# Kernel tuning notes

Measured on AMD Instinct MI355X. Metric: run time of the kernel, lower is better.

The kernel has to match this reference:

```python
import jax, jax.numpy as jnp
import numpy as np

N_HEADS = 8
N_POINTS = 4
EPS = 1e-5


def _conv1x1(x, w, b):
    # x: [B,C,H,W], w: [O,C]
    return jnp.einsum('bchw,oc->bohw', x, w) + b[None, :, None, None]


def _gn(x, g, b, groups=32):
    B, C, H, W = x.shape
    xr = x.reshape(B, groups, C // groups, H, W)
    m = xr.mean((2, 3, 4), keepdims=True)
    v = xr.var((2, 3, 4), keepdims=True)
    xn = ((xr - m) * jax.lax.rsqrt(v + EPS)).reshape(B, C, H, W)
    return xn * g[None, :, None, None] + b[None, :, None, None]


def _ln(x, g, b):
    m = x.mean(-1, keepdims=True)
    v = x.var(-1, keepdims=True)
    return (x - m) * jax.lax.rsqrt(v + EPS) * g + b


def _ln_spec(x, g2, b2, n):
    # modality-specific LayerNorm: separate params for v tokens [:n] and i tokens [n:]
    return jnp.concatenate([_ln(x[:, :n], g2[0], b2[0]), _ln(x[:, n:], g2[1], b2[1])], 1)


def _sine_pos(h, w, d):
    nf = d // 2
    scale = 2.0 * np.pi
    ye = jnp.arange(1, h + 1, dtype=jnp.float32) / h * scale
    xe = jnp.arange(1, w + 1, dtype=jnp.float32) / w * scale
    dim_t = 10000.0 ** (2.0 * (jnp.arange(nf) // 2).astype(jnp.float32) / nf)
    def enc(e):
        p = e[:, None] / dim_t
        return jnp.stack([jnp.sin(p[:, 0::2]), jnp.cos(p[:, 1::2])], -1).reshape(e.shape[0], nf)
    py = enc(ye)  # [h,nf]
    px = enc(xe)  # [w,nf]
    pos = jnp.concatenate([jnp.broadcast_to(py[:, None, :], (h, w, nf)),
                           jnp.broadcast_to(px[None, :, :], (h, w, nf))], -1)
    return pos.reshape(h * w, d)


def _bilinear(vl, loc):
    # vl: [B,h,w,Hd,Dh] value for one level, loc: [B,Lq,Hd,P,2] normalized (x,y)
    B, h, w, Hd, Dh = vl.shape
    Lq, P = loc.shape[1], loc.shape[3]
    x = loc[..., 0] * w - 0.5
    y = loc[..., 1] * h - 0.5
    x0 = jnp.floor(x)
    y0 = jnp.floor(y)
    wx = x - x0
    wy = y - y0
    x0i = x0.astype(jnp.int32)
    y0i = y0.astype(jnp.int32)
    v2 = vl.reshape(B, h * w, Hd, Dh).transpose(0, 2, 1, 3)  # [B,Hd,HW,Dh]
    def g(ix, iy):
        valid = ((ix >= 0) & (ix < w) & (iy >= 0) & (iy < h)).astype(vl.dtype)
        flat = jnp.clip(iy, 0, h - 1) * w + jnp.clip(ix, 0, w - 1)  # [B,Lq,Hd,P]
        idx = flat.transpose(0, 2, 1, 3).reshape(B, Hd, Lq * P)
        gv = jnp.take_along_axis(v2, idx[..., None], axis=2)  # [B,Hd,Lq*P,Dh]
        gv = gv.reshape(B, Hd, Lq, P, Dh).transpose(0, 2, 1, 3, 4)  # [B,Lq,Hd,P,Dh]
        return gv * valid[..., None]
    return (g(x0i, y0i) * ((1 - wx) * (1 - wy))[..., None]
            + g(x0i + 1, y0i) * (wx * (1 - wy))[..., None]
            + g(x0i, y0i + 1) * ((1 - wx) * wy)[..., None]
            + g(x0i + 1, y0i + 1) * (wx * wy)[..., None])


def _deform_attn(q, src, ref, shapes, ow, ob, aww, awb, vw, vb, opw, opb):
    B, Len, D = src.shape
    L = len(shapes)
    Hd, P = N_HEADS, N_POINTS
    Dh = D // Hd
    value = src @ vw + vb
    off = (q @ ow + ob).reshape(B, Len, Hd, L, P, 2)
    aw = jax.nn.softmax((q @ aww + awb).reshape(B, Len, Hd, L * P), -1).reshape(B, Len, Hd, L, P)
    norm = jnp.array([[s[1], s[0]] for s in shapes], jnp.float32)  # (w,h) per level
    loc = ref[None, :, None, None, None, :] + off / norm[None, None, None, :, None, :]
    out = jnp.zeros((B, Len, Hd, Dh), value.dtype)
    start = 0
    for l, (hh, ww) in enumerate(shapes):
        vl = value[:, start:start + hh * ww].reshape(B, hh, ww, Hd, Dh)
        samp = _bilinear(vl, loc[:, :, :, l])  # [B,Len,Hd,P,Dh]
        out = out + (samp * aw[:, :, :, l, :, None]).sum(3)
        start += hh * ww
    return out.reshape(B, Len, D) @ opw + opb


def _forward(input_v, input_i, av_w, av_b, av_g, av_be, ai_w, ai_b, ai_g, ai_be,
             level_embed, off_w, off_b, aw_w, aw_b, vp_w, vp_b, op_w, op_b,
             ln1_g, ln1_b, ffn1_w, ffn1_b, ffn2_w, ffn2_b, ln2_g, ln2_b,
             as_w, as_b, as_g, as_be):
    b, c, h, w = input_v.shape
    D = av_w.shape[0]
    hw = h * w
    fv = _gn(_conv1x1(input_v, av_w, av_b), av_g, av_be)
    fi = _gn(_conv1x1(input_i, ai_w, ai_b), ai_g, ai_be)
    sv = fv.reshape(b, D, hw).transpose(0, 2, 1)
    si = fi.reshape(b, D, hw).transpose(0, 2, 1)
    src = jnp.concatenate([sv, si], 1)  # [b, 2hw, D]
    pos = _sine_pos(h, w, D)
    posf = jnp.concatenate([pos + level_embed[0], pos + level_embed[1]], 0)
    gx = (jnp.arange(w, dtype=jnp.float32) + 0.5) / w
    gy = (jnp.arange(h, dtype=jnp.float32) + 0.5) / h
    X, Y = jnp.meshgrid(gx, gy)
    ref1 = jnp.stack([X, Y], -1).reshape(hw, 2)
    ref = jnp.concatenate([ref1, ref1], 0)  # [2hw, 2]
    shapes = [(h, w), (h, w)]
    for i in range(off_w.shape[0]):
        q = src + posf
        attn = _deform_attn(q, src, ref, shapes, off_w[i], off_b[i], aw_w[i], aw_b[i],
                            vp_w[i], vp_b[i], op_w[i], op_b[i])
        src = _ln_spec(src + attn, ln1_g[i], ln1_b[i], hw)
        ff = jax.nn.relu(src @ ffn1_w[i] + ffn1_b[i]) @ ffn2_w[i] + ffn2_b[i]
        src = _ln_spec(src + ff, ln2_g[i], ln2_b[i], hw)
    out = src[:, :hw] + src[:, hw:]  # chunk along tokens, sum modalities
    out = out.transpose(0, 2, 1).reshape(b, D, h, w)
    return _gn(_conv1x1(out, as_w, as_b), as_g, as_be)


def setup_inputs():
    key = jax.random.key(0)
    B, C, H, W = 16, 768, 20, 20
    D, NL, Hd, L, P, Dff = 512, 6, N_HEADS, 2, N_POINTS, 1024
    ks = iter(jax.random.split(key, 64))
    def rn(shape, scale=0.02):
        return jax.random.normal(next(ks), shape, jnp.float32) * scale
    return {
        'input_v': jax.random.normal(next(ks), (B, C, H, W), jnp.float32),
        'input_i': jax.random.normal(next(ks), (B, C, H, W), jnp.float32),
        'av_w': rn((D, C)), 'av_b': jnp.zeros((D,)), 'av_g': jnp.ones((D,)), 'av_be': jnp.zeros((D,)),
        'ai_w': rn((D, C)), 'ai_b': jnp.zeros((D,)), 'ai_g': jnp.ones((D,)), 'ai_be': jnp.zeros((D,)),
        'level_embed': rn((L, D)),
        'off_w': rn((NL, D, Hd * L * P * 2)), 'off_b': rn((NL, Hd * L * P * 2), 0.5),
        'aw_w': rn((NL, D, Hd * L * P)), 'aw_b': jnp.zeros((NL, Hd * L * P)),
        'vp_w': rn((NL, D, D)), 'vp_b': jnp.zeros((NL, D)),
        'op_w': rn((NL, D, D)), 'op_b': jnp.zeros((NL, D)),
        'ln1_g': jnp.ones((NL, 2, D)), 'ln1_b': jnp.zeros((NL, 2, D)),
        'ffn1_w': rn((NL, D, Dff)), 'ffn1_b': jnp.zeros((NL, Dff)),
        'ffn2_w': rn((NL, Dff, D)), 'ffn2_b': jnp.zeros((NL, D)),
        'ln2_g': jnp.ones((NL, 2, D)), 'ln2_b': jnp.zeros((NL, 2, D)),
        'as_w': rn((C, D)), 'as_b': jnp.zeros((C,)), 'as_g': jnp.ones((C,)), 'as_be': jnp.zeros((C,)),
    }


def reference(input_v, input_i, av_w, av_b, av_g, av_be, ai_w, ai_b, ai_g, ai_be,
              level_embed, off_w, off_b, aw_w, aw_b, vp_w, vp_b, op_w, op_b,
              ln1_g, ln1_b, ffn1_w, ffn1_b, ffn2_w, ffn2_b, ln2_g, ln2_b,
              as_w, as_b, as_g, as_be):
    return _forward(input_v, input_i, av_w, av_b, av_g, av_be, ai_w, ai_b, ai_g, ai_be,
                    level_embed, off_w, off_b, aw_w, aw_b, vp_w, vp_b, op_w, op_b,
                    ln1_g, ln1_b, ffn1_w, ffn1_b, ffn2_w, ffn2_b, ln2_g, ln2_b,
                    as_w, as_b, as_g, as_be)
```

## Files before the change

### kernel.cpp

```cpp
#include <hip/hip_runtime.h>
#include <hip/hip_bf16.h>
#include <cstddef>
#include <math.h>


constexpr int kB   = 16;
constexpr int kCin = 768;
constexpr int kHW  = 400;
constexpr int kWpx = 20;
constexpr int kHpx = 20;
constexpr int kD   = 512;
constexpr int kLen = 800;
constexpr int kDff = 1024;
constexpr int kNL  = 6;
constexpr float kEps = 1e-5f;

typedef __attribute__((ext_vector_type(8))) short s8v;
typedef __attribute__((ext_vector_type(4))) short s4v;
typedef __attribute__((ext_vector_type(4))) float f4v;

__device__ __forceinline__ int swzk(int row, int k) {
  return (k & ~31) | ((((k >> 3) + (row >> 1)) & 3) << 3) | (k & 7);
}

__device__ __forceinline__ unsigned short f2b(float f) {
  union { __hip_bfloat16 h; unsigned short u; } cv;
  cv.h = __float2bfloat16(f);
  return cv.u;
}

__device__ __forceinline__ float b2f(unsigned short u) {
  return __uint_as_float(((unsigned)u) << 16);
}

__device__ __forceinline__ void gll(const unsigned short* g, unsigned short* l) {
  __builtin_amdgcn_global_load_lds(
      (const __attribute__((address_space(1))) unsigned int*)g,
      (__attribute__((address_space(3))) unsigned int*)l, 16, 0, 0);
}

__device__ __forceinline__ void breduce2(float& s, float& s2, float* sh) {
#pragma unroll
  for (int o = 32; o > 0; o >>= 1) {
    s  += __shfl_down(s, o);
    s2 += __shfl_down(s2, o);
  }
  const int wid = threadIdx.x >> 6, lane = threadIdx.x & 63;
  if (lane == 0) { sh[wid] = s; sh[4 + wid] = s2; }
  __syncthreads();
  if (threadIdx.x == 0) {
    sh[0] = sh[0] + sh[1] + sh[2] + sh[3];
    sh[4] = sh[4] + sh[5] + sh[6] + sh[7];
  }
  __syncthreads();
  s = sh[0]; s2 = sh[4];
}

template<int EPI>
__global__ __launch_bounds__(256)
void mgemm(const unsigned short* __restrict__ Abf,
           const unsigned short* __restrict__ Bw,
           const float* __restrict__ bias,
           const unsigned short* __restrict__ resb,
           float* __restrict__ Cf, float* __restrict__ Cf2,
           const float* __restrict__ aux,
           unsigned short* __restrict__ Cb,
           int K, int ldc, int Nreal)
{
  __shared__ unsigned short As[3][4096];
  __shared__ unsigned short Bs[3][4096];
  const int tid = threadIdx.x;
  const int w = tid >> 6, l = tid & 63;
  const int m0 = blockIdx.y * 128;
  const int n0 = blockIdx.x * 128;

  if (EPI == 6 && m0 >= 6400) { Bw = resb; bias = aux; }

  f4v acc[4][4] = {};

  const int srow = w * 32 + (l >> 2);
  const unsigned short* ga0 = Abf + (size_t)(m0 + srow) * K + (l & 3) * 8;
  const unsigned short* ga1 = ga0 + (size_t)16 * K;
  const unsigned short* gb0 = Bw + (size_t)(n0 + srow) * K + (l & 3) * 8;
  const unsigned short* gb1 = gb0 + (size_t)16 * K;
  const int lb0 = (w * 32) * 32;
  const int lb1 = (w * 32 + 16) * 32;

  int aoff[4], boff[4];
#pragma unroll
  for (int f = 0; f < 4; f++) {
    const int ra = (w >> 1) * 64 + f * 16 + (l & 15);
    aoff[f] = ra * 32 + ((((l >> 4) + (ra >> 1)) & 3) << 3);
    const int rb = (w & 1) * 64 + f * 16 + (l & 15);
    boff[f] = rb * 32 + ((((l >> 4) + (rb >> 1)) & 3) << 3);
  }

#define STAGE(ko, bi) do { \
    gll(ga0 + (ko), &As[bi][lb0]); gll(ga1 + (ko), &As[bi][lb1]); \
    gll(gb0 + (ko), &Bs[bi][lb0]); gll(gb1 + (ko), &Bs[bi][lb1]); } while (0)

  const int NT = K >> 5;
  STAGE(0, 0);
  STAGE(32, 1);

  int cur = 0;
  int bpre = 2;
  int kpre = 64;
  for (int t = 0; t < NT; ++t) {
    if (t + 1 < NT) asm volatile("s_waitcnt vmcnt(4)" ::: "memory");
    else            asm volatile("s_waitcnt vmcnt(0)" ::: "memory");
    __builtin_amdgcn_s_barrier();
    __builtin_amdgcn_sched_barrier(0);
    if (t + 2 < NT) STAGE(kpre, bpre);
    s8v af[4], bf4[4];
#pragma unroll
    for (int f = 0; f < 4; f++) {
      af[f]  = *(const s8v*)&As[cur][aoff[f]];
      bf4[f] = *(const s8v*)&Bs[cur][boff[f]];
    }
#pragma unroll
    for (int i = 0; i < 4; i++)
#pragma unroll
      for (int j = 0; j < 4; j++)
        acc[i][j] = __builtin_amdgcn_mfma_f32_16x16x32_bf16(af[i], bf4[j], acc[i][j], 0, 0, 0);
    kpre += 32;
    bpre = (bpre == 2) ? 0 : bpre + 1;
    cur  = (cur == 2) ? 0 : cur + 1;
  }
#undef STAGE

  const int colb = n0 + (w & 1) * 64;
  const int rowb = m0 + (w >> 1) * 64 + (l >> 4) * 4;
#pragma unroll
  for (int i = 0; i < 4; i++) {
#pragma unroll
    for (int j = 0; j < 4; j++) {
      const int col = colb + j * 16 + (l & 15);
      float bv;
      if (EPI == 4) bv = (col < kD) ? bias[col] : 0.0f;
      else          bv = bias[col];
#pragma unroll
      for (int r = 0; r < 4; r++) {
        const int row = rowb + i * 16 + r;
        float v = acc[i][j][r] + bv;
        if (EPI == 1) {
          Cb[(size_t)row * ldc + swzk(row, col)] = f2b(fmaxf(v, 0.0f));
        } else if (EPI == 2) {
          v += b2f(resb[(size_t)row * kD + swzk(row, col)]);
          Cb[(size_t)row * kD + col] = f2b(v);
        } else if (EPI == 3) {
          const int bb = row / kHW, p = row % kHW;
          Cf[((size_t)bb * Nreal + col) * kHW + p] = v;
        } else if (EPI == 4) {
          if (col < kD) {
            Cb[(size_t)row * kD + col] = f2b(v);
          } else {
            const int c = col - kD;
            if (c < 192)
              Cf2[(size_t)row * 192 + c] = v + aux[(size_t)(row % kLen) * 192 + c];
          }
        } else if (EPI == 5) {
          if (row < kLen) {
            const int ll = col >> 8, c = col & 255;
            if (c < 192)
              Cf[(((size_t)ll * kLen) + row) * 192 + c] = v;
          }
        } else {
          Cb[(size_t)row * kD + col] = f2b(v);
        }
      }
    }
  }
}

__device__ __forceinline__ void cvt8t(const float* __restrict__ W,
                                      unsigned short* __restrict__ out,
                                      int K, int N, int g)
{
  const int n = g % N;
  const int k = (g / N) * 8;
  s8v p;
#pragma unroll
  for (int j = 0; j < 8; j++) p[j] = (short)f2b(W[(size_t)(k + j) * N + n]);
  const int base = n * K + (k & ~31) + ((((k >> 3) + (n >> 1)) & 3) << 3);
  *(s8v*)&out[base] = p;
}

__global__ __launch_bounds__(256)
void cvt_all_k(const float* __restrict__ vp_w, const float* __restrict__ op_w,
               const float* __restrict__ off_w, const float* __restrict__ aw_w,
               const float* __restrict__ f1w_a, const float* __restrict__ f2w_a,
               unsigned short* __restrict__ wall)
{
  const int lyr = blockIdx.x / 832;
  int g = (blockIdx.x % 832) * 256 + threadIdx.x;
  unsigned short* wl = wall + (size_t)lyr * 1703936;
  if (g < 32768) { cvt8t(vp_w + (size_t)lyr * kD * kD, wl, 512, 512, g); return; }
  g -= 32768;
  if (g < 16384) {
    const int n = g & 255;
    const int k = (g >> 8) * 8;
    const float* ow  = off_w + (size_t)lyr * kD * 128;
    const float* aww = aw_w  + (size_t)lyr * kD * 64;
    s8v p;
#pragma unroll
    for (int j = 0; j < 8; j++) {
      float v = 0.0f;
      if (n < 128)      v = ow[(size_t)(k + j) * 128 + n];
      else if (n < 192) v = aww[(size_t)(k + j) * 64 + (n - 128)];
      p[j] = (short)f2b(v);
    }
    const int row = 512 + n;
    const int base = row * 512 + (k & ~31) + ((((k >> 3) + (row >> 1)) & 3) << 3);
    *(s8v*)&wl[base] = p;
    return;
  }
  g -= 16384;
  if (g < 32768) { cvt8t(op_w + (size_t)lyr * kD * kD, wl + 393216, 512, 512, g); return; }
  g -= 32768;
  if (g < 65536) { cvt8t(f1w_a + (size_t)lyr * kD * kDff, wl + 655360, 512, 1024, g); return; }
  g -= 65536;
  cvt8t(f2w_a + (size_t)lyr * kDff * kD, wl + 1179648, 1024, 512, g);
}

__global__ __launch_bounds__(256)
void cvt_pre_k(const float* __restrict__ off_w, const float* __restrict__ aw_w,
               const float* __restrict__ off_b, const float* __restrict__ aw_b,
               unsigned short* __restrict__ woaw_all, float* __restrict__ biasall)
{
  int g = blockIdx.x * 256 + threadIdx.x;
  if (g < 98304) {
    const int l = g >> 14;
    const int gg = g & 16383;
    const int n = gg & 255;
    const int k = (gg >> 8) * 8;
    const float* ow = off_w + (size_t)l * kD * 128;
    const float* aww = aw_w + (size_t)l * kD * 64;
    s8v p;
#pragma unroll
    for (int j = 0; j < 8; j++) {
      float v = 0.0f;
      if (n < 128)      v = ow[(size_t)(k + j) * 128 + n];
      else if (n < 192) v = aww[(size_t)(k + j) * 64 + (n - 128)];
      p[j] = (short)f2b(v);
    }
    const int row = l * 256 + n;
    const int base = row * 512 + (k & ~31) + ((((k >> 3) + (row >> 1)) & 3) << 3);
    *(s8v*)&woaw_all[base] = p;
    return;
  }
  g -= 98304;
  const int l = g >> 8, c = g & 255;
  float v = 0.0f;
  if (c < 128)      v = off_b[l * 128 + c];
  else if (c < 192) v = aw_b[l * 64 + (c - 128)];
  biasall[l * 256 + c] = v;
}

__global__ void cvtw_d_k(const float* __restrict__ W, unsigned short* __restrict__ out,
                         int K, int N)
{
  const int gid = blockIdx.x * 256 + threadIdx.x;
  const int K8 = K >> 3;
  const int n  = gid / K8;
  const int k  = (gid % K8) * 8;
  s8v p;
#pragma unroll
  for (int j = 0; j < 8; j++) p[j] = (short)f2b(W[(size_t)n * K + k + j]);
  const int base = n * K + (k & ~31) + ((((k >> 3) + (n >> 1)) & 3) << 3);
  *(s8v*)&out[base] = p;
}

__global__ void cvtw_dd_k(const float* __restrict__ W0, const float* __restrict__ W1,
                          unsigned short* __restrict__ out)
{
  int gid = blockIdx.x * 256 + threadIdx.x;
  const float* W = W0;
  unsigned short* o = out;
  if (gid >= 49152) { gid -= 49152; W = W1; o = out + 393216; }
  const int n = gid / 96;
  const int k = (gid % 96) * 8;
  s8v p;
#pragma unroll
  for (int j = 0; j < 8; j++) p[j] = (short)f2b(W[(size_t)n * kCin + k + j]);
  const int base = n * kCin + (k & ~31) + ((((k >> 3) + (n >> 1)) & 3) << 3);
  *(s8v*)&o[base] = p;
}

__global__ void tin_k(const float* __restrict__ inv, const float* __restrict__ ini,
                      unsigned short* __restrict__ out)
{
  __shared__ float t[16][17];
  const int z = blockIdx.z;
  const int mod = z >> 4, b = z & 15;
  const float* in = (mod ? ini : inv) + (size_t)b * kCin * kHW;
  const int c0 = blockIdx.x * 16, p0 = blockIdx.y * 16;
  const int tx = threadIdx.x & 15, ty = threadIdx.x >> 4;
  t[ty][tx] = in[((size_t)(c0 + ty)) * kHW + p0 + tx];
  __syncthreads();
  const int row = z * kHW + p0 + ty;
  const int c = c0 + tx;
  out[(size_t)row * kCin + swzk(row, c)] = f2b(t[tx][ty]);
}

__global__ void posfb_k(unsigned short* __restrict__ posfb,
                        const float* __restrict__ level_embed)
{
  const int gid = blockIdx.x * 256 + threadIdx.x;
  const int d0 = (gid & 63) * 8;
  const int t  = gid >> 6;
  s8v o;
  if (t >= kLen) {
#pragma unroll
    for (int j = 0; j < 8; j++) o[j] = 0;
  } else {
    const int lvl = t / kHW;
    const int tt = t % kHW;
    const int yy = tt / kWpx, xx = tt % kWpx;
#pragma unroll
    for (int j = 0; j < 8; j++) {
      const int d = d0 + j;
      const int dd = d & 255;
      const float e = (d < 256) ? ((float)(yy + 1) * (6.283185307179586f / kHpx))
                                : ((float)(xx + 1) * (6.283185307179586f / kWpx));
      const float dimt = powf(10000.0f, (float)(dd >> 1) / 128.0f);
      const float pp = e / dimt;
      const float val = (dd & 1) ? cosf(pp) : sinf(pp);
      o[j] = (short)f2b(val + level_embed[lvl * kD + d]);
    }
  }
  *(s8v*)&posfb[(size_t)t * kD + swzk(t, d0)] = o;
}

__global__ __launch_bounds__(256)
void gn_stats_tok_k(const unsigned short* __restrict__ x, float* __restrict__ stats)
{
  __shared__ float sh[8];
  const int mb = blockIdx.x >> 5;
  const int g = blockIdx.x & 31;
  const unsigned short* xb = x + (size_t)mb * kHW * kD + g * 16;
  float s = 0.f, s2 = 0.f;
  for (int i = threadIdx.x; i < 800; i += 256) {
    const int p = i >> 1, half = i & 1;
    const s8v u = *(const s8v*)&xb[(size_t)p * kD + half * 8];
#pragma unroll
    for (int j = 0; j < 8; j++) {
      const float v = b2f((unsigned short)u[j]);
      s += v; s2 += v * v;
    }
  }
  breduce2(s, s2, sh);
  if (threadIdx.x == 0) {
    const float mean = s / (kHW * 16.0f);
    const float var  = s2 / (kHW * 16.0f) - mean * mean;
    stats[blockIdx.x * 2]     = mean;
    stats[blockIdx.x * 2 + 1] = rsqrtf(var + kEps);
  }
}

__global__ void gn_norm_tok_k(const unsigned short* __restrict__ x,
                              unsigned short* __restrict__ srcb,
                              const float* __restrict__ stats,
                              const float* __restrict__ gv, const float* __restrict__ bev,
                              const float* __restrict__ gi, const float* __restrict__ bei)
{
  const int gid = blockIdx.x * 256 + threadIdx.x;
  const int d0 = (gid & 63) * 8;
  const int rl = gid >> 6;
  const int mb = rl / kHW;
  const int p  = rl - mb * kHW;
  const int mod = mb >> 4, b = mb & 15;
  const int g = d0 >> 4;
  const float mean = stats[(mb * 32 + g) * 2];
  const float rstd = stats[(mb * 32 + g) * 2 + 1];
  const float* gam = mod ? gi : gv;
  const float* bet = mod ? bei : bev;
  const s8v u = *(const s8v*)&x[(size_t)rl * kD + d0];
  const int row = b * kLen + mod * kHW + p;
  s8v o;
#pragma unroll
  for (int j = 0; j < 8; j++)
    o[j] = (short)f2b((b2f((unsigned short)u[j]) - mean) * rstd * gam[d0 + j] + bet[d0 + j]);
  *(s8v*)&srcb[(size_t)row * kD + swzk(row, d0)] = o;
}

__global__ __launch_bounds__(256)
void gn_stats_ch_k(const float* __restrict__ x, float* __restrict__ stats)
{
  __shared__ float sh[8];
  const int b = blockIdx.x >> 5;
  const int g = blockIdx.x & 31;
  const float* xb = x + (size_t)b * kCin * kHW + (size_t)g * 24 * kHW;
  float s = 0.f, s2 = 0.f;
  for (int i = threadIdx.x; i < 24 * kHW; i += 256) {
    const float v = xb[i];
    s += v; s2 += v * v;
  }
  breduce2(s, s2, sh);
  if (threadIdx.x == 0) {
    const float mean = s / (24.0f * kHW);
    const float var  = s2 / (24.0f * kHW) - mean * mean;
    stats[blockIdx.x * 2]     = mean;
    stats[blockIdx.x * 2 + 1] = rsqrtf(var + kEps);
  }
}

__global__ void gn_norm_ch_k(const float* __restrict__ x, float* __restrict__ out,
                             const float* __restrict__ stats,
                             const float* __restrict__ gam, const float* __restrict__ bet)
{
  const int idx = blockIdx.x * 256 + threadIdx.x;
  const int rest = idx / kHW;
  const int c = rest % kCin;
  const int b = rest / kCin;
  const int g = c / 24;
  const float mean = stats[(b * 32 + g) * 2];
  const float rstd = stats[(b * 32 + g) * 2 + 1];
  out[idx] = (x[idx] - mean) * rstd * gam[c] + bet[c];
}

__global__ __launch_bounds__(256)
void ln4_k(const unsigned short* __restrict__ x, unsigned short* __restrict__ outb,
           const float* __restrict__ gamma, const float* __restrict__ beta)
{
  const int row = blockIdx.x * 4 + (threadIdx.x >> 6);
  const int l = threadIdx.x & 63;
  const int mod = ((row % kLen) < kHW) ? 0 : 1;
  const s8v u = *(const s8v*)&x[(size_t)row * kD + l * 8];
  float v[8];
#pragma unroll
  for (int j = 0; j < 8; j++) v[j] = b2f((unsigned short)u[j]);
  float s = 0.f, s2 = 0.f;
#pragma unroll
  for (int j = 0; j < 8; j++) { s += v[j]; s2 += v[j] * v[j]; }
#pragma unroll
  for (int o = 32; o > 0; o >>= 1) {
    s  += __shfl_xor(s, o);
    s2 += __shfl_xor(s2, o);
  }
  const float mean = s * (1.0f / kD);
  const float var  = s2 * (1.0f / kD) - mean * mean;
  const float rstd = rsqrtf(var + kEps);
  const float* g  = gamma + mod * kD + l * 8;
  const float* be = beta  + mod * kD + l * 8;
  s8v o8;
#pragma unroll
  for (int j = 0; j < 8; j++)
    o8[j] = (short)f2b((v[j] - mean) * rstd * g[j] + be[j]);
  *(s8v*)&outb[(size_t)row * kD + swzk(row, l * 8)] = o8;
}

__global__ __launch_bounds__(256)
void sample_k(const unsigned short* __restrict__ value, const float* __restrict__ offaw,
              unsigned short* __restrict__ out)
{
  __shared__ float wls[2][64][8];
  const int tid = threadIdx.x;
  const int tok = tid >> 7;
  const int wt  = tid & 127;
  const int token = blockIdx.x * 2 + tok;
  const int b = token / kLen;
  const int t = token % kLen;
  const int tt = t % kHW;

  if (wt < 64) {
    const int h = wt >> 3, lp = wt & 7, lvl = lp >> 2, p = lp & 3;
    const float* oa = offaw + (size_t)token * 192;
    const float lg = oa[128 + h * 8 + lp];
    float mx = lg;
#pragma unroll
    for (int msk = 1; msk < 8; msk <<= 1) mx = fmaxf(mx, __shfl_xor(mx, msk));
    const float ex = __expf(lg - mx);
    float ssum = ex;
#pragma unroll
    for (int msk = 1; msk < 8; msk <<= 1) ssum += __shfl_xor(ssum, msk);
    const float aw = ex / ssum;

    const float x = (float)(tt % kWpx) + oa[h * 16 + lvl * 8 + p * 2];
    const float y = (float)(tt / kWpx) + oa[h * 16 + lvl * 8 + p * 2 + 1];
    const float x0f = floorf(x), y0f = floorf(y);
    const float wx = x - x0f, wy = y - y0f;
    const int x0 = (int)x0f, y0 = (int)y0f;
    const int rowbase = b * kLen + lvl * kHW;
#pragma unroll
    for (int dy = 0; dy < 2; dy++) {
#pragma unroll
      for (int dx = 0; dx < 2; dx++) {
        const int ix = x0 + dx, iy = y0 + dy;
        const bool valid = (ix >= 0) & (ix < kWpx) & (iy >= 0) & (iy < kHpx);
        const float cw = (dx ? wx : 1.0f - wx) * (dy ? wy : 1.0f - wy);
        const float w = valid ? aw * cw : 0.0f;
        const int ixc = min(max(ix, 0), kWpx - 1);
        const int iyc = min(max(iy, 0), kHpx - 1);
        const int r = rowbase + iyc * kWpx + ixc;
        const int cn = dy * 2 + dx;
        wls[tok][wt][cn * 2]     = w;
        wls[tok][wt][cn * 2 + 1] = __int_as_float(r);
      }
    }
  }
  __syncthreads();

  const int c0 = wt * 4;
  const int h = wt >> 4;
  float acc0 = 0.f, acc1 = 0.f, acc2 = 0.f, acc3 = 0.f;
  const unsigned short* vb = value + c0;
#pragma unroll
  for (int pp = 0; pp < 8; pp++) {
    const float* wl = wls[tok][h * 8 + pp];
#pragma unroll
    for (int cn = 0; cn < 4; cn++) {
      const float w = wl[cn * 2];
      const int r = __float_as_int(wl[cn * 2 + 1]);
      const s4v q = *(const s4v*)(vb + (size_t)r * kD);
      acc0 += w * b2f((unsigned short)q[0]);
      acc1 += w * b2f((unsigned short)q[1]);
      acc2 += w * b2f((unsigned short)q[2]);
      acc3 += w * b2f((unsigned short)q[3]);
    }
  }
  const int sk = swzk(token, c0);
  s4v o;
  o[0] = (short)f2b(acc0); o[1] = (short)f2b(acc1);
  o[2] = (short)f2b(acc2); o[3] = (short)f2b(acc3);
  *(s4v*)&out[(size_t)token * kD + sk] = o;
}

__global__ void sumtok_k(const unsigned short* __restrict__ srcb,
                         unsigned short* __restrict__ tokb)
{
  const int gid = blockIdx.x * 256 + threadIdx.x;
  const int d0 = (gid & 63) * 8;
  const int rest = gid >> 6;
  const int b = rest / kHW, p = rest % kHW;
  const int r1 = b * kLen + p;
  const int r2 = r1 + kHW;
  const int ro = b * kHW + p;
  const s8v u1 = *(const s8v*)&srcb[(size_t)r1 * kD + swzk(r1, d0)];
  const s8v u2 = *(const s8v*)&srcb[(size_t)r2 * kD + swzk(r2, d0)];
  s8v o;
#pragma unroll
  for (int j = 0; j < 8; j++)
    o[j] = (short)f2b(b2f((unsigned short)u1[j]) + b2f((unsigned short)u2[j]));
  *(s8v*)&tokb[(size_t)ro * kD + swzk(ro, d0)] = o;
}

extern "C" void kernel_launch(void* const* d_in, const int* in_sizes, int n_in,
                              void* d_out, int out_size, void* d_ws, size_t ws_size,
                              hipStream_t stream)
{
  const float* input_v     = (const float*)d_in[0];
  const float* input_i     = (const float*)d_in[1];
  const float* av_w        = (const float*)d_in[2];
  const float* av_b        = (const float*)d_in[3];
  const float* av_g        = (const float*)d_in[4];
  const float* av_be       = (const float*)d_in[5];
  const float* ai_w        = (const float*)d_in[6];
  const float* ai_b        = (const float*)d_in[7];
  const float* ai_g        = (const float*)d_in[8];
  const float* ai_be       = (const float*)d_in[9];
  const float* level_embed = (const float*)d_in[10];
  const float* off_w       = (const float*)d_in[11];
  const float* off_b       = (const float*)d_in[12];
  const float* aw_w        = (const float*)d_in[13];
  const float* aw_b        = (const float*)d_in[14];
  const float* vp_w        = (const float*)d_in[15];
  const float* vp_b        = (const float*)d_in[16];
  const float* op_w        = (const float*)d_in[17];
  const float* op_b        = (const float*)d_in[18];
  const float* ln1_g       = (const float*)d_in[19];
  const float* ln1_b       = (const float*)d_in[20];
  const float* ffn1_w      = (const float*)d_in[21];
  const float* ffn1_b      = (const float*)d_in[22];
  const float* ffn2_w      = (const float*)d_in[23];
  const float* ffn2_b      = (const float*)d_in[24];
  const float* ln2_g       = (const float*)d_in[25];
  const float* ln2_b       = (const float*)d_in[26];
  const float* as_w        = (const float*)d_in[27];
  const float* as_b        = (const float*)d_in[28];
  const float* as_g        = (const float*)d_in[29];
  const float* as_be       = (const float*)d_in[30];

  float* wsf     = (float*)d_ws;
  float* offaw   = wsf;
  float* posWc   = offaw   + (size_t)2457600;
  float* biasall = posWc   + (size_t)921600;
  float* stats   = biasall + (size_t)1536;
  unsigned short* srcb     = (unsigned short*)(stats + 2048);
  unsigned short* bufA     = srcb     + (size_t)6553600;
  unsigned short* bufB     = bufA     + (size_t)13107200;
  unsigned short* wall     = bufB     + (size_t)6553600;
  unsigned short* wcs      = wall     + (size_t)10223616;
  unsigned short* woaw_all = wcs      + (size_t)786432;
  unsigned short* posfb    = woaw_all + (size_t)786432;
  float* wallf = (float*)wall;

  const int M = kB * kLen;

  posfb_k<<<dim3(224), 256, 0, stream>>>(posfb, level_embed);
  cvt_pre_k<<<dim3(390), 256, 0, stream>>>(off_w, aw_w, off_b, aw_b,
                                           woaw_all, biasall);
  mgemm<5><<<dim3(12, 7), 256, 0, stream>>>(
      posfb, woaw_all, biasall, nullptr, posWc, nullptr, nullptr, nullptr,
      512, 0, 0);

  tin_k<<<dim3(48, 25, 32), 256, 0, stream>>>(input_v, input_i, bufA);
  cvtw_dd_k<<<dim3(384), 256, 0, stream>>>(av_w, ai_w, wcs);
  mgemm<6><<<dim3(4, 100), 256, 0, stream>>>(
      bufA, wcs, av_b, wcs + 393216, nullptr, nullptr, ai_b, bufB, 768, 512, 0);
  gn_stats_tok_k<<<dim3(1024), 256, 0, stream>>>(bufB, stats);
  gn_norm_tok_k<<<dim3(3200), 256, 0, stream>>>(
      bufB, srcb, stats, av_g, av_be, ai_g, ai_be);

  cvt_all_k<<<dim3(4992), 256, 0, stream>>>(vp_w, op_w, off_w, aw_w,
                                            ffn1_w, ffn2_w, wall);

  for (int l = 0; l < kNL; l++) {
    unsigned short* wcomb = wall + (size_t)l * 1703936;
    unsigned short* wop   = wcomb + 393216;
    unsigned short* wf1   = wcomb + 655360;
    unsigned short* wf2   = wcomb + 1179648;
    const float* vbl  = vp_b   + (size_t)l * kD;
    const float* opbl = op_b   + (size_t)l * kD;
    const float* l1g  = ln1_g  + (size_t)l * 2 * kD;
    const float* l1b  = ln1_b  + (size_t)l * 2 * kD;
    const float* f1b  = ffn1_b + (size_t)l * kDff;
    const float* f2b_ = ffn2_b + (size_t)l * kD;
    const float* l2g  = ln2_g  + (size_t)l * 2 * kD;
    const float* l2b  = ln2_b  + (size_t)l * 2 * kD;

    mgemm<4><<<dim3(6, 100), 256, 0, stream>>>(
        srcb, wcomb, vbl, nullptr, nullptr, offaw, posWc + (size_t)l * 153600,
        bufA, 512, 0, 0);

    sample_k<<<dim3(M / 2), 256, 0, stream>>>(bufA, offaw, bufB);

    mgemm<2><<<dim3(4, 100), 256, 0, stream>>>(
        bufB, wop, opbl, srcb, nullptr, nullptr, nullptr, bufA, 512, 512, 0);

    ln4_k<<<dim3(M / 4), 256, 0, stream>>>(bufA, srcb, l1g, l1b);

    mgemm<1><<<dim3(8, 100), 256, 0, stream>>>(
        srcb, wf1, f1b, nullptr, nullptr, nullptr, nullptr, bufA, 512, 1024, 0);
    mgemm<2><<<dim3(4, 100), 256, 0, stream>>>(
        bufA, wf2, f2b_, srcb, nullptr, nullptr, nullptr, bufB, 1024, 512, 0);

    ln4_k<<<dim3(M / 4), 256, 0, stream>>>(bufB, srcb, l2g, l2b);
  }

  sumtok_k<<<dim3(1600), 256, 0, stream>>>(srcb, bufA);
  cvtw_d_k<<<dim3(192), 256, 0, stream>>>(as_w, wcs, 512, 768);
  mgemm<3><<<dim3(6, 50), 256, 0, stream>>>(
      bufA, wcs, as_b, nullptr, wallf, nullptr, nullptr, nullptr, 512, 0, 768);
  gn_stats_ch_k<<<dim3(kB * 32), 256, 0, stream>>>(wallf, stats);
  gn_norm_ch_k<<<dim3(19200), 256, 0, stream>>>(
      wallf, (float*)d_out, stats, as_g, as_be);
}
```

Measured before the change: 1.098 ms.

## Remap GEMM blocks per XCD, raise MFMA priority, store offsets in bf16, merge prep kernels

Several unrelated changes land together. GEMM workgroup IDs are remapped so consecutive tiles run on the same XCD, and s_setprio wraps the MFMA loop. The sampling offsets and attention logits are written as bf16 instead of fp32, which halves that traffic but costs precision in the sampling coordinates. Separate preprocessing kernels (pos/embed, weight conversion, input transpose) are merged into fewer launches.

```diff
diff --git a/kernel.cpp b/kernel.cpp
--- a/kernel.cpp
+++ b/kernel.cpp
@@ -62,7 +62,7 @@
            const unsigned short* __restrict__ Bw,
            const float* __restrict__ bias,
            const unsigned short* __restrict__ resb,
-           float* __restrict__ Cf, float* __restrict__ Cf2,
+           float* __restrict__ Cf, unsigned short* __restrict__ Cb2,
            const float* __restrict__ aux,
            unsigned short* __restrict__ Cb,
            int K, int ldc, int Nreal)
@@ -71,8 +71,15 @@
   __shared__ unsigned short Bs[3][4096];
   const int tid = threadIdx.x;
   const int w = tid >> 6, l = tid & 63;
-  const int m0 = blockIdx.y * 128;
-  const int n0 = blockIdx.x * 128;
+
+  const int gx = gridDim.x;
+  const int nwg = gx * gridDim.y;
+  const int bid = blockIdx.y * gx + blockIdx.x;
+  const int q = nwg >> 3, r = nwg & 7;
+  const int xcd = bid & 7, idx = bid >> 3;
+  const int wgid = (xcd < r ? xcd * (q + 1) : r * (q + 1) + (xcd - r) * q) + idx;
+  const int m0 = (wgid / gx) * 128;
+  const int n0 = (wgid % gx) * 128;
 
   if (EPI == 6 && m0 >= 6400) { Bw = resb; bias = aux; }
 
@@ -118,11 +125,13 @@
       af[f]  = *(const s8v*)&As[cur][aoff[f]];
       bf4[f] = *(const s8v*)&Bs[cur][boff[f]];
     }
+    __builtin_amdgcn_s_setprio(1);
 #pragma unroll
     for (int i = 0; i < 4; i++)
 #pragma unroll
       for (int j = 0; j < 4; j++)
         acc[i][j] = __builtin_amdgcn_mfma_f32_16x16x32_bf16(af[i], bf4[j], acc[i][j], 0, 0, 0);
+    __builtin_amdgcn_s_setprio(0);
     kpre += 32;
     bpre = (bpre == 2) ? 0 : bpre + 1;
     cur  = (cur == 2) ? 0 : cur + 1;
@@ -140,9 +149,9 @@
       if (EPI == 4) bv = (col < kD) ? bias[col] : 0.0f;
       else          bv = bias[col];
 #pragma unroll
-      for (int r = 0; r < 4; r++) {
-        const int row = rowb + i * 16 + r;
-        float v = acc[i][j][r] + bv;
+      for (int r2 = 0; r2 < 4; r2++) {
+        const int row = rowb + i * 16 + r2;
+        float v = acc[i][j][r2] + bv;
         if (EPI == 1) {
           Cb[(size_t)row * ldc + swzk(row, col)] = f2b(fmaxf(v, 0.0f));
         } else if (EPI == 2) {
@@ -157,7 +166,7 @@
           } else {
             const int c = col - kD;
             if (c < 192)
-              Cf2[(size_t)row * 192 + c] = v + aux[(size_t)(row % kLen) * 192 + c];
+              Cb2[(size_t)row * 192 + c] = f2b(v + aux[(size_t)(row % kLen) * 192 + c]);
           }
         } else if (EPI == 5) {
           if (row < kLen) {
@@ -224,11 +233,40 @@
 }
 
 __global__ __launch_bounds__(256)
-void cvt_pre_k(const float* __restrict__ off_w, const float* __restrict__ aw_w,
-               const float* __restrict__ off_b, const float* __restrict__ aw_b,
-               unsigned short* __restrict__ woaw_all, float* __restrict__ biasall)
+void pre_k(const float* __restrict__ level_embed,
+           const float* __restrict__ off_w, const float* __restrict__ aw_w,
+           const float* __restrict__ off_b, const float* __restrict__ aw_b,
+           unsigned short* __restrict__ posfb,
+           unsigned short* __restrict__ woaw_all, float* __restrict__ biasall)
 {
   int g = blockIdx.x * 256 + threadIdx.x;
+  if (g < 57344) {
+    const int d0 = (g & 63) * 8;
+    const int t  = g >> 6;
+    s8v o;
+    if (t >= kLen) {
+#pragma unroll
+      for (int j = 0; j < 8; j++) o[j] = 0;
+    } else {
+      const int lvl = t / kHW;
+      const int tt = t % kHW;
+      const int yy = tt / kWpx, xx = tt % kWpx;
+#pragma unroll
+      for (int j = 0; j < 8; j++) {
+        const int d = d0 + j;
+        const int dd = d & 255;
+        const float e = (d < 256) ? ((float)(yy + 1) * (6.283185307179586f / kHpx))
+                                  : ((float)(xx + 1) * (6.283185307179586f / kWpx));
+        const float dimt = powf(10000.0f, (float)(dd >> 1) / 128.0f);
+        const float pp = e / dimt;
+        const float val = (dd & 1) ? cosf(pp) : sinf(pp);
+        o[j] = (short)f2b(val + level_embed[lvl * kD + d]);
+      }
+    }
+    *(s8v*)&posfb[(size_t)t * kD + swzk(t, d0)] = o;
+    return;
+  }
+  g -= 57344;
   if (g < 98304) {
     const int l = g >> 14;
     const int gg = g & 16383;
@@ -250,11 +288,13 @@
     return;
   }
   g -= 98304;
-  const int l = g >> 8, c = g & 255;
-  float v = 0.0f;
-  if (c < 128)      v = off_b[l * 128 + c];
-  else if (c < 192) v = aw_b[l * 64 + (c - 128)];
-  biasall[l * 256 + c] = v;
+  if (g < 1536) {
+    const int l = g >> 8, c = g & 255;
+    float v = 0.0f;
+    if (c < 128)      v = off_b[l * 128 + c];
+    else if (c < 192) v = aw_b[l * 64 + (c - 128)];
+    biasall[l * 256 + c] = v;
+  }
 }
 
 __global__ void cvtw_d_k(const float* __restrict__ W, unsigned short* __restrict__ out,
@@ -271,13 +311,30 @@
   *(s8v*)&out[base] = p;
 }
 
-__global__ void cvtw_dd_k(const float* __restrict__ W0, const float* __restrict__ W1,
-                          unsigned short* __restrict__ out)
-{
-  int gid = blockIdx.x * 256 + threadIdx.x;
+__global__ void tincvt_k(const float* __restrict__ inv, const float* __restrict__ ini,
+                         const float* __restrict__ W0, const float* __restrict__ W1,
+                         unsigned short* __restrict__ out, unsigned short* __restrict__ wcs)
+{
+  __shared__ float t[16][17];
+  const int bid = blockIdx.x;
+  if (bid < 38400) {
+    const int z = bid / 1200;
+    const int rem = bid % 1200;
+    const int c0 = (rem % 48) * 16, p0 = (rem / 48) * 16;
+    const int mod = z >> 4, b = z & 15;
+    const float* in = (mod ? ini : inv) + (size_t)b * kCin * kHW;
+    const int tx = threadIdx.x & 15, ty = threadIdx.x >> 4;
+    t[ty][tx] = in[((size_t)(c0 + ty)) * kHW + p0 + tx];
+    __syncthreads();
+    const int row = z * kHW + p0 + ty;
+    const int c = c0 + tx;
+    out[(size_t)row * kCin + swzk(row, c)] = f2b(t[tx][ty]);
+    return;
+  }
+  int gid = (bid - 38400) * 256 + threadIdx.x;
   const float* W = W0;
-  unsigned short* o = out;
-  if (gid >= 49152) { gid -= 49152; W = W1; o = out + 393216; }
+  unsigned short* o = wcs;
+  if (gid >= 49152) { gid -= 49152; W = W1; o = wcs + 393216; }
   const int n = gid / 96;
   const int k = (gid % 96) * 8;
   s8v p;
@@ -285,51 +342,6 @@
   for (int j = 0; j < 8; j++) p[j] = (short)f2b(W[(size_t)n * kCin + k + j]);
   const int base = n * kCin + (k & ~31) + ((((k >> 3) + (n >> 1)) & 3) << 3);
   *(s8v*)&o[base] = p;
-}
-
-__global__ void tin_k(const float* __restrict__ inv, const float* __restrict__ ini,
-                      unsigned short* __restrict__ out)
-{
-  __shared__ float t[16][17];
-  const int z = blockIdx.z;
-  const int mod = z >> 4, b = z & 15;
-  const float* in = (mod ? ini : inv) + (size_t)b * kCin * kHW;
-  const int c0 = blockIdx.x * 16, p0 = blockIdx.y * 16;
-  const int tx = threadIdx.x & 15, ty = threadIdx.x >> 4;
-  t[ty][tx] = in[((size_t)(c0 + ty)) * kHW + p0 + tx];
-  __syncthreads();
-  const int row = z * kHW + p0 + ty;
-  const int c = c0 + tx;
-  out[(size_t)row * kCin + swzk(row, c)] = f2b(t[tx][ty]);
-}
-
-__global__ void posfb_k(unsigned short* __restrict__ posfb,
-                        const float* __restrict__ level_embed)
-{
-  const int gid = blockIdx.x * 256 + threadIdx.x;
-  const int d0 = (gid & 63) * 8;
-  const int t  = gid >> 6;
-  s8v o;
-  if (t >= kLen) {
-#pragma unroll
-    for (int j = 0; j < 8; j++) o[j] = 0;
-  } else {
-    const int lvl = t / kHW;
-    const int tt = t % kHW;
-    const int yy = tt / kWpx, xx = tt % kWpx;
-#pragma unroll
-    for (int j = 0; j < 8; j++) {
-      const int d = d0 + j;
-      const int dd = d & 255;
-      const float e = (d < 256) ? ((float)(yy + 1) * (6.283185307179586f / kHpx))
-                                : ((float)(xx + 1) * (6.283185307179586f / kWpx));
-      const float dimt = powf(10000.0f, (float)(dd >> 1) / 128.0f);
-      const float pp = e / dimt;
-      const float val = (dd & 1) ? cosf(pp) : sinf(pp);
-      o[j] = (short)f2b(val + level_embed[lvl * kD + d]);
-    }
-  }
-  *(s8v*)&posfb[(size_t)t * kD + swzk(t, d0)] = o;
 }
 
 __global__ __launch_bounds__(256)
@@ -451,7 +463,8 @@
 }
 
 __global__ __launch_bounds__(256)
-void sample_k(const unsigned short* __restrict__ value, const float* __restrict__ offaw,
+void sample_k(const unsigned short* __restrict__ value,
+              const unsigned short* __restrict__ offaw,
               unsigned short* __restrict__ out)
 {
   __shared__ float wls[2][64][8];
@@ -465,8 +478,8 @@
 
   if (wt < 64) {
     const int h = wt >> 3, lp = wt & 7, lvl = lp >> 2, p = lp & 3;
-    const float* oa = offaw + (size_t)token * 192;
-    const float lg = oa[128 + h * 8 + lp];
+    const unsigned short* oa = offaw + (size_t)token * 192;
+    const float lg = b2f(oa[128 + h * 8 + lp]);
     float mx = lg;
 #pragma unroll
     for (int msk = 1; msk < 8; msk <<= 1) mx = fmaxf(mx, __shfl_xor(mx, msk));
@@ -476,8 +489,8 @@
     for (int msk = 1; msk < 8; msk <<= 1) ssum += __shfl_xor(ssum, msk);
     const float aw = ex / ssum;
 
-    const float x = (float)(tt % kWpx) + oa[h * 16 + lvl * 8 + p * 2];
-    const float y = (float)(tt / kWpx) + oa[h * 16 + lvl * 8 + p * 2 + 1];
+    const float x = (float)(tt % kWpx) + b2f(oa[h * 16 + lvl * 8 + p * 2]);
+    const float y = (float)(tt / kWpx) + b2f(oa[h * 16 + lvl * 8 + p * 2 + 1]);
     const float x0f = floorf(x), y0f = floorf(y);
     const float wx = x - x0f, wy = y - y0f;
     const int x0 = (int)x0f, y0 = (int)y0f;
@@ -581,9 +594,8 @@
   const float* as_g        = (const float*)d_in[29];
   const float* as_be       = (const float*)d_in[30];
 
-  float* wsf     = (float*)d_ws;
-  float* offaw   = wsf;
-  float* posWc   = offaw   + (size_t)2457600;
+  unsigned short* offawb = (unsigned short*)d_ws;
+  float* posWc   = (float*)(offawb + 2457600);
   float* biasall = posWc   + (size_t)921600;
   float* stats   = biasall + (size_t)1536;
   unsigned short* srcb     = (unsigned short*)(stats + 2048);
@@ -597,15 +609,14 @@
 
   const int M = kB * kLen;
 
-  posfb_k<<<dim3(224), 256, 0, stream>>>(posfb, level_embed);
-  cvt_pre_k<<<dim3(390), 256, 0, stream>>>(off_w, aw_w, off_b, aw_b,
-                                           woaw_all, biasall);
+  pre_k<<<dim3(614), 256, 0, stream>>>(level_embed, off_w, aw_w, off_b, aw_b,
+                                       posfb, woaw_all, biasall);
   mgemm<5><<<dim3(12, 7), 256, 0, stream>>>(
       posfb, woaw_all, biasall, nullptr, posWc, nullptr, nullptr, nullptr,
       512, 0, 0);
 
-  tin_k<<<dim3(48, 25, 32), 256, 0, stream>>>(input_v, input_i, bufA);
-  cvtw_dd_k<<<dim3(384), 256, 0, stream>>>(av_w, ai_w, wcs);
+  tincvt_k<<<dim3(38784), 256, 0, stream>>>(input_v, input_i, av_w, ai_w,
+                                            bufA, wcs);
   mgemm<6><<<dim3(4, 100), 256, 0, stream>>>(
       bufA, wcs, av_b, wcs + 393216, nullptr, nullptr, ai_b, bufB, 768, 512, 0);
   gn_stats_tok_k<<<dim3(1024), 256, 0, stream>>>(bufB, stats);
@@ -630,10 +641,10 @@
     const float* l2b  = ln2_b  + (size_t)l * 2 * kD;
 
     mgemm<4><<<dim3(6, 100), 256, 0, stream>>>(
-        srcb, wcomb, vbl, nullptr, nullptr, offaw, posWc + (size_t)l * 153600,
+        srcb, wcomb, vbl, nullptr, nullptr, offawb, posWc + (size_t)l * 153600,
         bufA, 512, 0, 0);
 
-    sample_k<<<dim3(M / 2), 256, 0, stream>>>(bufA, offaw, bufB);
+    sample_k<<<dim3(M / 2), 256, 0, stream>>>(bufA, offawb, bufB);
 
     mgemm<2><<<dim3(4, 100), 256, 0, stream>>>(
         bufB, wop, opbl, srcb, nullptr, nullptr, nullptr, bufA, 512, 512, 0);
```

Result: no change. 1.085 ms (-1.2%).
